# Optimization experiments

Measured on AMD Instinct MI355X. Metric: run time of the kernel, lower is better.

## Reference

```python
import jax, jax.numpy as jnp
import numpy as np

N = 50000      # nodes in batched graph
E = 800000     # edges
IN_DIM = 16
HID = 64
NH = 4         # heads
G = 128        # graphs in batch
OUT_DIM = 32
NUM_LAYERS = 8
NEG_SLOPE = 0.2  # DGL GATv2Conv default


def setup_inputs() -> dict:
    key = jax.random.key(0)
    ks = jax.random.split(key, 12)
    feat = jax.random.normal(ks[0], (N, IN_DIM), dtype=jnp.float32)
    src = jax.random.randint(ks[1], (E,), 0, N, dtype=jnp.int32)
    dst = jax.random.randint(ks[2], (E,), 0, N, dtype=jnp.int32)
    graph_ids = jnp.sort(jax.random.randint(ks[3], (N,), 0, G, dtype=jnp.int32))
    is_root = jax.random.randint(ks[4], (N,), 0, 2, dtype=jnp.int32)
    s_in = 1.0 / np.sqrt(IN_DIM)
    s_h = 1.0 / np.sqrt(2 * HID)
    s_o = 1.0 / np.sqrt(HID)
    return {
        'feat': feat, 'src': src, 'dst': dst,
        'graph_ids': graph_ids, 'is_root': is_root,
        'W_in': jax.random.normal(ks[5], (IN_DIM, HID), jnp.float32) * s_in,
        'b_in': jnp.zeros((HID,), jnp.float32),
        'W_src': jax.random.normal(ks[6], (2 * HID, NH * HID), jnp.float32) * s_h,
        'b_src': jnp.zeros((NH * HID,), jnp.float32),
        'W_dst': jax.random.normal(ks[7], (2 * HID, NH * HID), jnp.float32) * s_h,
        'b_dst': jnp.zeros((NH * HID,), jnp.float32),
        'attn': jax.random.normal(ks[8], (NH, HID), jnp.float32) * s_o,
        'W_out': jax.random.normal(ks[9], (HID, OUT_DIM), jnp.float32) * s_o,
        'b_out': jnp.zeros((OUT_DIM,), jnp.float32),
    }


def reference(feat, src, dst, graph_ids, is_root,
              W_in, b_in, W_src, b_src, W_dst, b_dst, attn, W_out, b_out):
    h0 = feat @ W_in + b_in                       # [N, HID]
    h = h0
    for _ in range(NUM_LAYERS):
        x = jnp.concatenate([h, h0], axis=1)      # [N, 2*HID]
        fs = (x @ W_src + b_src).reshape(-1, NH, HID)  # [N, NH, HID]
        fd = (x @ W_dst + b_dst).reshape(-1, NH, HID)
        # per-edge GATv2 attention logits
        e = jax.nn.leaky_relu(fs[src] + fd[dst], NEG_SLOPE)   # [E, NH, HID]
        s = jnp.einsum('ehd,hd->eh', e, attn)                 # [E, NH]
        # segment softmax over incoming edges of each dst node
        m = jax.ops.segment_max(s, dst, num_segments=N)       # [N, NH]
        a = jnp.exp(s - m[dst])
        denom = jax.ops.segment_sum(a, dst, num_segments=N)
        alpha = a / denom[dst]                                # [E, NH]
        # weighted aggregation of source features
        agg = jax.ops.segment_sum(alpha[:, :, None] * fs[src], dst,
                                  num_segments=N)             # [N, NH, HID]
        h = jnp.tanh(agg).sum(axis=1)                         # [N, HID]
    # root-weighted readout per graph
    hg = jax.ops.segment_sum(h * is_root.astype(h.dtype)[:, None],
                             graph_ids, num_segments=G)       # [G, HID]
    return hg @ W_out + b_out                                 # [G, OUT_DIM]
```

## Files before the change

### kernel.cpp

```cpp
#include <hip/hip_runtime.h>
#include <math.h>

#define N_NODES 50000
#define N_EDGES 800000
#define IN_DIM  16
#define HID     64
#define NH      4
#define NGRAPH  128
#define OUT_DIM 32
#define NUM_LAYERS 8
#define NEG_SLOPE 0.2f

#define SCAN_BLOCKS ((N_NODES + 255) / 256)

typedef unsigned short u16;
typedef unsigned char  u8;
typedef _Float16 h2   __attribute__((ext_vector_type(2)));
typedef _Float16 f16x8 __attribute__((ext_vector_type(8)));
typedef float f32x2 __attribute__((ext_vector_type(2)));
typedef __attribute__((ext_vector_type(4))) float f32x4;

static __device__ __forceinline__ u16 f2h(float f) {
    _Float16 h = (_Float16)f; u16 r; __builtin_memcpy(&r, &h, 2); return r;
}
static __device__ __forceinline__ float h2f_lo(unsigned w) {
    _Float16 h; u16 u = (u16)w; __builtin_memcpy(&h, &u, 2); return (float)h;
}
static __device__ __forceinline__ h2 shfl_h2(h2 v, int mask) {
    int i; __builtin_memcpy(&i, &v, 4); i = __shfl_xor(i, mask);
    h2 r; __builtin_memcpy(&r, &i, 4); return r;
}
static __device__ __forceinline__ h2 bcast_h2(float f) {
    _Float16 h = (_Float16)f; h2 r; r[0] = h; r[1] = h; return r;
}
static __device__ __forceinline__ h2 pkrtz_h2(float a, float b) {
    auto v = __builtin_amdgcn_cvt_pkrtz(a, b);
    h2 r; __builtin_memcpy(&r, &v, 4); return r;
}

#define DPP_XOR1(x) __uint_as_float((unsigned)__builtin_amdgcn_update_dpp(0, (int)__float_as_uint(x), 0xB1, 0xF, 0xF, true))
#define DPP_XOR2(x) __uint_as_float((unsigned)__builtin_amdgcn_update_dpp(0, (int)__float_as_uint(x), 0x4E, 0xF, 0xF, true))


__global__ void k_build_wpack(const float* __restrict__ Wsrc, const float* __restrict__ bsrc,
                              const float* __restrict__ Wdst, const float* __restrict__ bdst,
                              const float* __restrict__ attn,
                              u16* __restrict__ Wpack, float* __restrict__ bcat,
                              u16* __restrict__ an_h) {
    int tid = blockIdx.x * 256 + threadIdx.x;
    int i = tid & 7;
    int l = (tid >> 3) & 63;
    int rest = tid >> 9;
    int kt = rest & 3;
    int nt = rest >> 2;
    int k = kt * 32 + (l >> 4) * 8 + i;
    int col = nt * 16 + (l & 15);
    float v = (col < 256) ? Wsrc[k * 256 + col] : Wdst[k * 256 + (col - 256)];
    Wpack[tid] = f2h(v);
    if (tid < 512) bcat[tid] = (tid < 256) ? bsrc[tid] : bdst[tid - 256];
    if (tid < 256) an_h[tid] = f2h(attn[tid] * 1.44269504f);
}

__global__ void k_hist(const int* __restrict__ dst, int* __restrict__ deg) {
    int e = blockIdx.x * 256 + threadIdx.x;
    if (e < N_EDGES) atomicAdd(&deg[dst[e]], 1);
}

__global__ void k_blocksum(const int* __restrict__ deg, int* __restrict__ bsum) {
    __shared__ int sm[256];
    int i = blockIdx.x * 256 + threadIdx.x;
    sm[threadIdx.x] = (i < N_NODES) ? deg[i] : 0;
    __syncthreads();
    for (int s = 128; s > 0; s >>= 1) {
        if (threadIdx.x < s) sm[threadIdx.x] += sm[threadIdx.x + s];
        __syncthreads();
    }
    if (threadIdx.x == 0) bsum[blockIdx.x] = sm[0];
}

__global__ void k_scanbsum(int* __restrict__ bsum) {
    if (threadIdx.x == 0 && blockIdx.x == 0) {
        int acc = 0;
        for (int b = 0; b < SCAN_BLOCKS; b++) { int t = bsum[b]; bsum[b] = acc; acc += t; }
    }
}

__global__ void k_rowptr(const int* __restrict__ deg, const int* __restrict__ bsum,
                         int* __restrict__ row_ptr) {
    __shared__ int sm[256];
    int i = blockIdx.x * 256 + threadIdx.x;
    int v = (i < N_NODES) ? deg[i] : 0;
    sm[threadIdx.x] = v;
    __syncthreads();
    for (int s = 1; s < 256; s <<= 1) {
        int t = (threadIdx.x >= (unsigned)s) ? sm[threadIdx.x - s] : 0;
        __syncthreads();
        sm[threadIdx.x] += t;
        __syncthreads();
    }
    if (i < N_NODES) row_ptr[i] = bsum[blockIdx.x] + sm[threadIdx.x] - v;
}

__global__ void k_scatter(const int* __restrict__ src, const int* __restrict__ dst,
                          const int* __restrict__ row_ptr, int* __restrict__ cursor,
                          int* __restrict__ csr_src) {
    int e = blockIdx.x * 256 + threadIdx.x;
    if (e < N_EDGES) {
        int d = dst[e];
        int pos = atomicAdd(&cursor[d], 1);
        csr_src[row_ptr[d] + pos] = src[e];
    }
}

__global__ __launch_bounds__(256) void k_in_gemm(const float* __restrict__ feat,
                                                 const float* __restrict__ W,
                                                 const float* __restrict__ b,
                                                 u16* __restrict__ h0h) {
    __shared__ float sW[IN_DIM * HID];
    __shared__ float sb[HID];
    int t = threadIdx.x;
    for (int i = t; i < IN_DIM * HID; i += 256) sW[i] = W[i];
    if (t < HID) sb[t] = b[t];
    __syncthreads();
    int wid = (blockIdx.x * 256 + t) >> 6;
    int lane = t & 63;
    const float* f = feat + wid * IN_DIM;
    float acc = sb[lane];
    #pragma unroll
    for (int k = 0; k < IN_DIM; k++) acc += f[k] * sW[k * HID + lane];
    h0h[wid * HID + lane] = f2h(acc);
}


#define ST_STRIDE 152
__global__ __launch_bounds__(256) void k_gemm_mfma(const u16* __restrict__ hb,
                                                   const u16* __restrict__ h0b,
                                                   const u16* __restrict__ Wpack,
                                                   const float* __restrict__ bcat,
                                                   u8* __restrict__ fs8,
                                                   u16* __restrict__ fdh) {
    __shared__ u16 sW[16384];
    __shared__ u16 sStage[4][2432];
    int tid = threadIdx.x;
    int g  = blockIdx.x & 3;
    int tb = blockIdx.x >> 2;
    int l = tid & 63, w = tid >> 6;
    int lr = l & 15, lg = l >> 4;

    {
        const f16x8* src = (const f16x8*)(Wpack + g * 16384);
        f16x8* dst = (f16x8*)sW;
        #pragma unroll
        for (int it = 0; it < 8; it++) dst[it * 256 + tid] = src[it * 256 + tid];
    }
    __syncthreads();

    size_t row0 = (size_t)(tb * 4 + w) * 16;
    if (row0 >= N_NODES) return;

    f32x4 acc[8];
    #pragma unroll
    for (int nt = 0; nt < 8; nt++) acc[nt] = (f32x4){0.f, 0.f, 0.f, 0.f};

    #pragma unroll
    for (int kt = 0; kt < 4; kt++) {
        const u16* A = (kt < 2) ? hb : h0b;
        f16x8 a = *(const f16x8*)(A + (row0 + lr) * HID + (kt & 1) * 32 + lg * 8);
        #pragma unroll
        for (int nt = 0; nt < 8; nt++) {
            f16x8 bfr = *(const f16x8*)(sW + nt * 2048 + kt * 512 + l * 8);
            acc[nt] = __builtin_amdgcn_mfma_f32_16x16x32_f16(a, bfr, acc[nt], 0, 0, 0);
        }
    }

    u16* myst = sStage[w];
    #pragma unroll
    for (int nt = 0; nt < 8; nt++) {
        float bv = bcat[g * 128 + nt * 16 + lr];
        #pragma unroll
        for (int j = 0; j < 4; j++)
            myst[(lg * 4 + j) * ST_STRIDE + nt * 16 + lr] = f2h(acc[nt][j] + bv);
    }
    #pragma unroll
    for (int j = 0; j < 4; j++) {
        int rloc = j * 4 + lg;
        f16x8 v = *(const f16x8*)(myst + rloc * ST_STRIDE + lr * 8);
        if (g < 2) {
            int p0 = __builtin_amdgcn_cvt_pk_fp8_f32((float)v[0], (float)v[1], 0, false);
            int p1 = __builtin_amdgcn_cvt_pk_fp8_f32((float)v[2], (float)v[3], 0, false);
            int p2 = __builtin_amdgcn_cvt_pk_fp8_f32((float)v[4], (float)v[5], 0, false);
            int p3 = __builtin_amdgcn_cvt_pk_fp8_f32((float)v[6], (float)v[7], 0, false);
            uint2 o8;
            o8.x = (unsigned)(p0 & 0xffff) | ((unsigned)p1 << 16);
            o8.y = (unsigned)(p2 & 0xffff) | ((unsigned)p3 << 16);
            *(uint2*)(fs8 + (row0 + rloc) * 256 + g * 128 + lr * 8) = o8;
        } else {
            *(f16x8*)(fdh + (row0 + rloc) * 256 + (g - 2) * 128 + lr * 8) = v;
        }
    }
}

__global__ __launch_bounds__(256) void k_edge(const u8* __restrict__ fs8,
                                              const u16* __restrict__ fdh,
                                              const u16* __restrict__ an_h,
                                              const int* __restrict__ row_ptr,
                                              const int* __restrict__ deg,
                                              const int* __restrict__ csr_src,
                                              u16* __restrict__ h) {
    int wid = (blockIdx.x * 256 + threadIdx.x) >> 6;
    int lane = threadIdx.x & 63;
    int g  = lane >> 4;
    int ll = lane & 15;
    const size_t ebase = (size_t)ll * 16;

    h2 an[8], fdhv[8];
    {
        const uint4* ap = (const uint4*)(an_h + ebase);
        uint4 a0 = ap[0], a1 = ap[1];
        unsigned aw[8] = {a0.x, a0.y, a0.z, a0.w, a1.x, a1.y, a1.z, a1.w};
        __builtin_memcpy(an, aw, 32);
        const uint4* fp = (const uint4*)(fdh + (size_t)wid * 256 + ebase);
        uint4 b0 = fp[0], b1 = fp[1];
        unsigned fw[8] = {b0.x, b0.y, b0.z, b0.w, b1.x, b1.y, b1.z, b1.w};
        __builtin_memcpy(fdhv, fw, 32);
    }
    const h2 slope2 = {(_Float16)NEG_SLOPE, (_Float16)NEG_SLOPE};

    float m = -3.0e38f, denom = 0.f;
    h2 agg[8];
    #pragma unroll
    for (int q = 0; q < 8; q++) agg[q] = (h2){(_Float16)0.f, (_Float16)0.f};

    int r0 = row_ptr[wid], dg = deg[wid];
    for (int i = g; i < dg; i += 4) {
        int s = csr_src[r0 + i];
        uint4 A = *(const uint4*)(fs8 + (size_t)s * 256 + ebase);

        h2 f[8];
        {
            unsigned d[4] = {A.x, A.y, A.z, A.w};
            #pragma unroll
            for (int q = 0; q < 4; q++) {
                f32x2 lo = __builtin_amdgcn_cvt_pk_f32_fp8((int)d[q], false);
                f32x2 hi = __builtin_amdgcn_cvt_pk_f32_fp8((int)d[q], true);
                f[2*q]   = pkrtz_h2(lo[0], lo[1]);
                f[2*q+1] = pkrtz_h2(hi[0], hi[1]);
            }
        }
        float p0 = 0.f, p1 = 0.f;
        #pragma unroll
        for (int q = 0; q < 8; q += 2) {
            h2 e0 = f[q]   + fdhv[q];
            h2 e1 = f[q+1] + fdhv[q+1];
            h2 l0 = __builtin_elementwise_max(e0, e0 * slope2);
            h2 l1 = __builtin_elementwise_max(e1, e1 * slope2);
            p0 = __builtin_amdgcn_fdot2(l0, an[q],   p0, false);
            p1 = __builtin_amdgcn_fdot2(l1, an[q+1], p1, false);
        }
        float p = p0 + p1;
        p += DPP_XOR1(p);
        p += DPP_XOR2(p);

        float c;
        if (__builtin_expect(p > m + 4.f, 0)) {
            float rs = exp2f(m - p);
            h2 rs2 = bcast_h2(rs);
            #pragma unroll
            for (int q = 0; q < 8; q++) agg[q] = agg[q] * rs2;
            denom *= rs;
            m = p;
            c = 1.f;
        } else {
            c = exp2f(p - m);
        }
        h2 c2 = bcast_h2(c);
        #pragma unroll
        for (int q = 0; q < 8; q++) agg[q] = agg[q] + f[q] * c2;
        denom += c;
    }

    {
        float mm = fmaxf(m, __shfl_xor(m, 16));
        mm = fmaxf(mm, __shfl_xor(mm, 32));
        float sc = exp2f(m - mm);
        denom *= sc;
        h2 sc2 = bcast_h2(sc);
        #pragma unroll
        for (int q = 0; q < 8; q++) agg[q] = agg[q] * sc2;
        denom += __shfl_xor(denom, 16);
        denom += __shfl_xor(denom, 32);
        #pragma unroll
        for (int q = 0; q < 8; q++) {
            agg[q] = agg[q] + shfl_h2(agg[q], 16);
            agg[q] = agg[q] + shfl_h2(agg[q], 32);
        }
    }

    float inv = denom > 0.f ? __builtin_amdgcn_rcpf(denom) : 0.f;
    float inv2 = inv * 2.885390082f;

    h2 x0 = (g & 2) ? ((g & 1) ? agg[6] : agg[4]) : ((g & 1) ? agg[2] : agg[0]);
    h2 x1 = (g & 2) ? ((g & 1) ? agg[7] : agg[5]) : ((g & 1) ? agg[3] : agg[1]);
    float t[4] = {(float)x0[0], (float)x0[1], (float)x1[0], (float)x1[1]};
    #pragma unroll
    for (int j = 0; j < 4; j++) {
        float E = exp2f(t[j] * inv2);
        float r = __builtin_amdgcn_rcpf(E + 1.f);
        float v = fmaf(-2.f, r, 1.f);
        v += __shfl_xor(v, 4);
        v += __shfl_xor(v, 8);
        t[j] = v;
    }
    if (ll < 4) {
        uint2 o;
        o.x = (unsigned)f2h(t[0]) | ((unsigned)f2h(t[1]) << 16);
        o.y = (unsigned)f2h(t[2]) | ((unsigned)f2h(t[3]) << 16);
        *(uint2*)(h + (size_t)wid * 64 + ll * 16 + g * 4) = o;
    }
}


__global__ __launch_bounds__(256) void k_readout(const u16* __restrict__ h,
                                                 const int* __restrict__ graph_ids,
                                                 const int* __restrict__ is_root,
                                                 float* __restrict__ hg) {
    int wid = (blockIdx.x * 256 + threadIdx.x) >> 6;
    int lane = threadIdx.x & 63;
    if (is_root[wid]) {
        int g = graph_ids[wid];
        atomicAdd(&hg[g * HID + lane], h2f_lo(h[(size_t)wid * HID + lane]));
    }
}

__global__ void k_out_gemm(const float* __restrict__ hg, const float* __restrict__ W,
                           const float* __restrict__ b, float* __restrict__ out) {
    int i = blockIdx.x * 256 + threadIdx.x;
    if (i >= NGRAPH * OUT_DIM) return;
    int g = i >> 5, o = i & 31;
    float acc = b[o];
    #pragma unroll
    for (int k = 0; k < HID; k++) acc += hg[g * HID + k] * W[k * OUT_DIM + o];
    out[i] = acc;
}


extern "C" void kernel_launch(void* const* d_in, const int* in_sizes, int n_in,
                              void* d_out, int out_size, void* d_ws, size_t ws_size,
                              hipStream_t stream) {
    const float* feat      = (const float*)d_in[0];
    const int*   src       = (const int*)d_in[1];
    const int*   dst       = (const int*)d_in[2];
    const int*   graph_ids = (const int*)d_in[3];
    const int*   is_root   = (const int*)d_in[4];
    const float* W_in      = (const float*)d_in[5];
    const float* b_in      = (const float*)d_in[6];
    const float* W_src     = (const float*)d_in[7];
    const float* b_src     = (const float*)d_in[8];
    const float* W_dst     = (const float*)d_in[9];
    const float* b_dst     = (const float*)d_in[10];
    const float* attn      = (const float*)d_in[11];
    const float* W_out     = (const float*)d_in[12];
    const float* b_out     = (const float*)d_in[13];
    float* out = (float*)d_out;

    char* base = (char*)d_ws;
    size_t off = 0;
    auto carve = [&](size_t bytes) -> char* {
        char* p = base + off;
        off = (off + bytes + 255) & ~(size_t)255;
        return p;
    };
    u16*   h0b     = (u16*)carve((size_t)N_NODES * HID * 2);
    u16*   hb      = (u16*)carve((size_t)N_NODES * HID * 2);
    u8*    fs8     = (u8*)carve((size_t)N_NODES * 256);
    u16*   fdh     = (u16*)carve((size_t)N_NODES * 256 * 2);
    u16*   Wpack   = (u16*)carve(128 * 512 * 2);
    float* bcat    = (float*)carve(512 * 4);
    u16*   an_h    = (u16*)carve(256 * 2);
    int*   csr_src = (int*)carve((size_t)N_EDGES * 4);
    int*   row_ptr = (int*)carve((size_t)N_NODES * 4);
    int*   bsum    = (int*)carve(SCAN_BLOCKS * 4);
    char*  zero0   = carve(0);
    int*   deg     = (int*)carve((size_t)N_NODES * 4);
    int*   cursor  = (int*)carve((size_t)N_NODES * 4);
    float* hg      = (float*)carve((size_t)NGRAPH * HID * 4);
    char*  zero1   = base + off;
    if (off > ws_size) return;

    (void)hipMemsetAsync(zero0, 0, (size_t)(zero1 - zero0), stream);

    k_build_wpack<<<256, 256, 0, stream>>>(W_src, b_src, W_dst, b_dst, attn, Wpack, bcat, an_h);
    k_hist<<<(N_EDGES + 255) / 256, 256, 0, stream>>>(dst, deg);
    k_blocksum<<<SCAN_BLOCKS, 256, 0, stream>>>(deg, bsum);
    k_scanbsum<<<1, 64, 0, stream>>>(bsum);
    k_rowptr<<<SCAN_BLOCKS, 256, 0, stream>>>(deg, bsum, row_ptr);
    k_scatter<<<(N_EDGES + 255) / 256, 256, 0, stream>>>(src, dst, row_ptr, cursor, csr_src);

    k_in_gemm<<<N_NODES / 4, 256, 0, stream>>>(feat, W_in, b_in, h0b);

    const int gemm_grid = ((N_NODES / 16 + 3) / 4) * 4;
    for (int layer = 0; layer < NUM_LAYERS; layer++) {
        const u16* hcur = (layer == 0) ? h0b : hb;
        k_gemm_mfma<<<gemm_grid, 256, 0, stream>>>(hcur, h0b, Wpack, bcat, fs8, fdh);
        k_edge<<<N_NODES / 4, 256, 0, stream>>>(fs8, fdh, an_h, row_ptr, deg, csr_src, hb);
    }

    k_readout<<<N_NODES / 4, 256, 0, stream>>>(hb, graph_ids, is_root, hg);
    k_out_gemm<<<(NGRAPH * OUT_DIM + 255) / 256, 256, 0, stream>>>(hg, W_out, b_out, out);
}
```

Measured before the change: 824.1 us.

## Store source features as fp16 and prefetch next edge's gather

```diff
diff --git a/kernel.cpp b/kernel.cpp
--- a/kernel.cpp
+++ b/kernel.cpp
@@ -32,10 +32,6 @@
 }
 static __device__ __forceinline__ h2 bcast_h2(float f) {
     _Float16 h = (_Float16)f; h2 r; r[0] = h; r[1] = h; return r;
-}
-static __device__ __forceinline__ h2 pkrtz_h2(float a, float b) {
-    auto v = __builtin_amdgcn_cvt_pkrtz(a, b);
-    h2 r; __builtin_memcpy(&r, &v, 4); return r;
 }
 
 #define DPP_XOR1(x) __uint_as_float((unsigned)__builtin_amdgcn_update_dpp(0, (int)__float_as_uint(x), 0xB1, 0xF, 0xF, true))
@@ -137,7 +133,7 @@
                                                    const u16* __restrict__ h0b,
                                                    const u16* __restrict__ Wpack,
                                                    const float* __restrict__ bcat,
-                                                   u8* __restrict__ fs8,
+                                                   u16* __restrict__ fsh,
                                                    u16* __restrict__ fdh) {
     __shared__ u16 sW[16384];
     __shared__ u16 sStage[4][2432];
@@ -181,26 +177,17 @@
         for (int j = 0; j < 4; j++)
             myst[(lg * 4 + j) * ST_STRIDE + nt * 16 + lr] = f2h(acc[nt][j] + bv);
     }
+    u16* dsth = (g < 2) ? fsh : fdh;
+    int colh = (g & 1) * 128;
     #pragma unroll
     for (int j = 0; j < 4; j++) {
         int rloc = j * 4 + lg;
         f16x8 v = *(const f16x8*)(myst + rloc * ST_STRIDE + lr * 8);
-        if (g < 2) {
-            int p0 = __builtin_amdgcn_cvt_pk_fp8_f32((float)v[0], (float)v[1], 0, false);
-            int p1 = __builtin_amdgcn_cvt_pk_fp8_f32((float)v[2], (float)v[3], 0, false);
-            int p2 = __builtin_amdgcn_cvt_pk_fp8_f32((float)v[4], (float)v[5], 0, false);
-            int p3 = __builtin_amdgcn_cvt_pk_fp8_f32((float)v[6], (float)v[7], 0, false);
-            uint2 o8;
-            o8.x = (unsigned)(p0 & 0xffff) | ((unsigned)p1 << 16);
-            o8.y = (unsigned)(p2 & 0xffff) | ((unsigned)p3 << 16);
-            *(uint2*)(fs8 + (row0 + rloc) * 256 + g * 128 + lr * 8) = o8;
-        } else {
-            *(f16x8*)(fdh + (row0 + rloc) * 256 + (g - 2) * 128 + lr * 8) = v;
-        }
-    }
-}
-
-__global__ __launch_bounds__(256) void k_edge(const u8* __restrict__ fs8,
+        *(f16x8*)(dsth + (row0 + rloc) * 256 + colh + lr * 8) = v;
+    }
+}
+
+__global__ __launch_bounds__(256) void k_edge(const u16* __restrict__ fsh,
                                               const u16* __restrict__ fdh,
                                               const u16* __restrict__ an_h,
                                               const int* __restrict__ row_ptr,
@@ -232,20 +219,25 @@
     for (int q = 0; q < 8; q++) agg[q] = (h2){(_Float16)0.f, (_Float16)0.f};
 
     int r0 = row_ptr[wid], dg = deg[wid];
+
+    uint4 A0 = {0,0,0,0}, A1 = {0,0,0,0};
+    if (g < dg) {
+        int s = csr_src[r0 + g];
+        const uint4* P = (const uint4*)(fsh + (size_t)s * 256 + ebase);
+        A0 = P[0]; A1 = P[1];
+    }
+
     for (int i = g; i < dg; i += 4) {
-        int s = csr_src[r0 + i];
-        uint4 A = *(const uint4*)(fs8 + (size_t)s * 256 + ebase);
+        int inext = i + 4;
+        bool hN = inext < dg;
+        int sN = csr_src[r0 + (hN ? inext : i)];
+        const uint4* PN = (const uint4*)(fsh + (size_t)sN * 256 + ebase);
+        uint4 B0 = PN[0], B1 = PN[1];
 
         h2 f[8];
         {
-            unsigned d[4] = {A.x, A.y, A.z, A.w};
-            #pragma unroll
-            for (int q = 0; q < 4; q++) {
-                f32x2 lo = __builtin_amdgcn_cvt_pk_f32_fp8((int)d[q], false);
-                f32x2 hi = __builtin_amdgcn_cvt_pk_f32_fp8((int)d[q], true);
-                f[2*q]   = pkrtz_h2(lo[0], lo[1]);
-                f[2*q+1] = pkrtz_h2(hi[0], hi[1]);
-            }
+            unsigned fw[8] = {A0.x, A0.y, A0.z, A0.w, A1.x, A1.y, A1.z, A1.w};
+            __builtin_memcpy(f, fw, 32);
         }
         float p0 = 0.f, p1 = 0.f;
         #pragma unroll
@@ -277,6 +269,8 @@
         #pragma unroll
         for (int q = 0; q < 8; q++) agg[q] = agg[q] + f[q] * c2;
         denom += c;
+
+        A0 = B0; A1 = B1;
     }
 
     {
@@ -372,7 +366,7 @@
     };
     u16*   h0b     = (u16*)carve((size_t)N_NODES * HID * 2);
     u16*   hb      = (u16*)carve((size_t)N_NODES * HID * 2);
-    u8*    fs8     = (u8*)carve((size_t)N_NODES * 256);
+    u16*   fsh     = (u16*)carve((size_t)N_NODES * 256 * 2);
     u16*   fdh     = (u16*)carve((size_t)N_NODES * 256 * 2);
     u16*   Wpack   = (u16*)carve(128 * 512 * 2);
     float* bcat    = (float*)carve(512 * 4);
@@ -401,8 +395,8 @@
     const int gemm_grid = ((N_NODES / 16 + 3) / 4) * 4;
     for (int layer = 0; layer < NUM_LAYERS; layer++) {
         const u16* hcur = (layer == 0) ? h0b : hb;
-        k_gemm_mfma<<<gemm_grid, 256, 0, stream>>>(hcur, h0b, Wpack, bcat, fs8, fdh);
-        k_edge<<<N_NODES / 4, 256, 0, stream>>>(fs8, fdh, an_h, row_ptr, deg, csr_src, hb);
+        k_gemm_mfma<<<gemm_grid, 256, 0, stream>>>(hcur, h0b, Wpack, bcat, fsh, fdh);
+        k_edge<<<N_NODES / 4, 256, 0, stream>>>(fsh, fdh, an_h, row_ptr, deg, csr_src, hb);
     }
 
     k_readout<<<N_NODES / 4, 256, 0, stream>>>(hb, graph_ids, is_root, hg);
```

Result: slower. 862.7 us (+4.7%).
